# Kernel optimization log

Hardware: AMD Instinct MI355X
Metric: run time of the kernel (lower is better)

## Reference

```python
import jax, jax.numpy as jnp
import numpy as np

LS = 16000      # FFT length = ceil(L/stride)*stride with L=16000, stride=128
STRIDE = 128    # decimation hop
B, C, L, K = 32, 40, 16000, 128


def setup_inputs() -> dict:
    key = jax.random.key(0)
    k1, k2, k3 = jax.random.split(key, 3)
    x = jax.random.normal(k1, (B, 1, L), dtype=jnp.float32)
    kernels_real = jax.random.normal(k2, (C, K), dtype=jnp.float32)
    kernels_imag = jax.random.normal(k3, (C, K), dtype=jnp.float32)
    return {"x": x, "kernels_real": kernels_real, "kernels_imag": kernels_imag}


def reference(x, kernels_real, kernels_imag):
    # Complex analysis filters (C, K); zero-padded to LS inside fft via n=LS
    kernels = kernels_real + 1j * kernels_imag
    Xf = jnp.fft.fft(x, n=LS, axis=-1)                     # (B, 1, LS) complex
    Kf = jnp.fft.fft(kernels, n=LS, axis=-1)[None, :, :]   # (1, C, LS) complex
    y = jnp.fft.ifft(Xf * Kf, n=LS, axis=-1)               # (B, C, LS) circular conv
    return y[:, :, ::STRIDE]                               # (B, C, LS//STRIDE) complex
```

## Files before the change

kernel.cpp:

```cpp
#include <hip/hip_runtime.h>

#define BB     32
#define CC     40
#define LL     16000
#define KK     128
#define MM     125
#define KPAD   129
#define NOUT   (BB * CC * MM)

__global__ __launch_bounds__(256) void ISAC_conv_kernel(
    const float* __restrict__ x,
    const float* __restrict__ kr,
    const float* __restrict__ ki,
    float*       __restrict__ out,
    int mode)
{
    __shared__ unsigned int skc[CC * KPAD];

    for (int i = threadIdx.x; i < CC * KK; i += 256) {
        int c = i >> 7;
        int k = i & 127;
        unsigned int br = __float_as_uint(kr[i]);
        unsigned int bi = __float_as_uint(ki[i]);
        unsigned int hr = (br + 0x7FFFu + ((br >> 16) & 1u)) & 0xFFFF0000u;
        unsigned int hi = (bi + 0x7FFFu + ((bi >> 16) & 1u)) >> 16;
        skc[c * KPAD + k] = hr | hi;
    }
    __syncthreads();

    int id = blockIdx.x * 256 + threadIdx.x;
    int c  = id % CC;
    int t  = id / CC;
    int m  = t % MM;
    int b  = t / MM;

    const unsigned int* kc = skc + c * KPAD;
    const float*        xb = x + b * LL;
    const int base = m * KK;

    const float* p = xb + (m == 0 ? LL : base);

    unsigned int u0 = kc[0];
    float xv0  = xb[base];
    float accr = xv0 * __uint_as_float(u0 & 0xFFFF0000u);
    float acci = xv0 * __uint_as_float(u0 << 16);

#pragma unroll
    for (int j = 1; j < KK; ++j) {
        float        xv = p[-j];
        unsigned int u  = kc[j];
        accr = fmaf(xv, __uint_as_float(u & 0xFFFF0000u), accr);
        acci = fmaf(xv, __uint_as_float(u << 16),         acci);
    }

    int oidx = (b * CC + c) * MM + m;
    if (mode == 0) {
        out[oidx]        = accr;
        out[NOUT + oidx] = acci;
    } else if (mode == 1) {
        out[oidx] = accr;
    } else {
        reinterpret_cast<float2*>(out)[oidx] = make_float2(accr, acci);
    }
}

extern "C" void kernel_launch(void* const* d_in, const int* in_sizes, int n_in,
                              void* d_out, int out_size, void* d_ws, size_t ws_size,
                              hipStream_t stream) {
    const float* x  = (const float*)d_in[0];
    const float* kr = (const float*)d_in[1];
    const float* ki = (const float*)d_in[2];
    float* out = (float*)d_out;

    int mode;
    if (out_size == 2 * NOUT)      mode = 0;
    else if (out_size == NOUT)     mode = 1;
    else                           mode = 2;

    const int total = NOUT;
    const int block = 256;
    const int grid  = (total + block - 1) / block;

    ISAC_conv_kernel<<<grid, block, 0, stream>>>(x, kr, ki, out, mode);
}
```

Before: 62.72 us.

## Recast strided convolution as bf16 MFMA GEMM with hi/lo split of input

Adds a prep kernel that gathers each output's 128-sample window of x into a row matrix, splitting it into bf16 high and low parts, and packs both filter banks into a bf16 column matrix. A second kernel runs 16x16x32 bf16 MFMA tiles over these matrices and scatters results to the real and imaginary output planes. This replaces the per-thread scalar FMA loop with matrix-core work, at the cost of an extra kernel launch and workspace traffic. The path is taken only when the output is in split layout and enough workspace is provided.

```diff
diff --git a/kernel.cpp b/kernel.cpp
--- a/kernel.cpp
+++ b/kernel.cpp
@@ -7,6 +7,94 @@
 #define MM     125
 #define KPAD   129
 #define NOUT   (BB * CC * MM)
+#define RTOT   (BB * MM)
+#define NCOL   (2 * CC)
+#define NTILE  ((RTOT / 16) * (NCOL / 16))
+
+using short8 = __attribute__((ext_vector_type(8))) short;
+using f32x4  = __attribute__((ext_vector_type(4))) float;
+
+__device__ __forceinline__ unsigned int bf16_rne(float v) {
+    unsigned int u = __float_as_uint(v);
+    return (u + 0x7FFFu + ((u >> 16) & 1u)) >> 16;
+}
+
+__global__ __launch_bounds__(256) void ISAC_prep(
+    const float* __restrict__ x,
+    const float* __restrict__ kr,
+    const float* __restrict__ ki,
+    unsigned int* __restrict__ whi,
+    unsigned int* __restrict__ wlo,
+    unsigned int* __restrict__ wkb)
+{
+    int bid = blockIdx.x;
+    if (bid < 1000) {
+        int pid = bid * 256 + threadIdx.x;
+        int r  = pid >> 6;
+        int kp = pid & 63;
+        int b  = r / MM;
+        int m  = r - b * MM;
+        int i0 = m * KK - 2 * kp;  if (i0 < 0) i0 += LL;
+        int i1 = i0 - 1;           if (i1 < 0) i1 += LL;
+        float xa = x[b * LL + i0];
+        float xb = x[b * LL + i1];
+        unsigned int ha = bf16_rne(xa), hb = bf16_rne(xb);
+        float la = xa - __uint_as_float(ha << 16);
+        float lb = xb - __uint_as_float(hb << 16);
+        whi[pid] = ha | (hb << 16);
+        wlo[pid] = bf16_rne(la) | (bf16_rne(lb) << 16);
+    } else {
+        int pid = (bid - 1000) * 256 + threadIdx.x;
+        if (pid < NCOL * 64) {
+            int col = pid >> 6;
+            int kp  = pid & 63;
+            const float* src = (col < CC) ? (kr + col * KK) : (ki + (col - CC) * KK);
+            wkb[pid] = bf16_rne(src[2 * kp]) | (bf16_rne(src[2 * kp + 1]) << 16);
+        }
+    }
+}
+
+__global__ __launch_bounds__(256) void ISAC_gemm(
+    const unsigned short* __restrict__ whi,
+    const unsigned short* __restrict__ wlo,
+    const unsigned short* __restrict__ wkb,
+    float* __restrict__ out)
+{
+    int tile = blockIdx.x * 4 + (threadIdx.x >> 6);
+    if (tile >= NTILE) return;
+    int lane = threadIdx.x & 63;
+    int rt = tile / 5;
+    int ct = tile - rt * 5;
+    int row = lane & 15;
+    int g   = lane >> 4;
+
+    const short8* pa = (const short8*)(whi + ((rt * 16 + row) * KK + g * 8));
+    const short8* pl = (const short8*)(wlo + ((rt * 16 + row) * KK + g * 8));
+    const short8* pb = (const short8*)(wkb + ((ct * 16 + row) * KK + g * 8));
+
+    f32x4 acc = {0.f, 0.f, 0.f, 0.f};
+#pragma unroll
+    for (int ks = 0; ks < 4; ++ks) {
+        short8 ah = pa[ks * 4];
+        short8 al = pl[ks * 4];
+        short8 bv = pb[ks * 4];
+        acc = __builtin_amdgcn_mfma_f32_16x16x32_bf16(ah, bv, acc, 0, 0, 0);
+        acc = __builtin_amdgcn_mfma_f32_16x16x32_bf16(al, bv, acc, 0, 0, 0);
+    }
+
+    int colIdx = ct * 16 + row;
+    int rbase  = rt * 16 + g * 4;
+#pragma unroll
+    for (int e = 0; e < 4; ++e) {
+        int rr = rbase + e;
+        int b  = rr / MM;
+        int m  = rr - b * MM;
+        int oidx = (colIdx < CC)
+                 ? ((b * CC + colIdx) * MM + m)
+                 : (NOUT + (b * CC + (colIdx - CC)) * MM + m);
+        out[oidx] = acc[e];
+    }
+}
 
 __global__ __launch_bounds__(256) void ISAC_conv_kernel(
     const float* __restrict__ x,
@@ -37,7 +125,6 @@
     const unsigned int* kc = skc + c * KPAD;
     const float*        xb = x + b * LL;
     const int base = m * KK;
-
     const float* p = xb + (m == 0 ? LL : base);
 
     unsigned int u0 = kc[0];
@@ -77,9 +164,17 @@
     else if (out_size == NOUT)     mode = 1;
     else                           mode = 2;
 
-    const int total = NOUT;
-    const int block = 256;
-    const int grid  = (total + block - 1) / block;
-
-    ISAC_conv_kernel<<<grid, block, 0, stream>>>(x, kr, ki, out, mode);
+    const size_t ws_need = (size_t)(256000 + 256000 + 5120) * 4;
+    if (mode == 0 && d_ws != nullptr && ws_size >= ws_need) {
+        unsigned int* whi = (unsigned int*)d_ws;
+        unsigned int* wlo = whi + 256000;
+        unsigned int* wkb = wlo + 256000;
+        ISAC_prep<<<1020, 256, 0, stream>>>(x, kr, ki, whi, wlo, wkb);
+        ISAC_gemm<<<(NTILE + 3) / 4, 256, 0, stream>>>(
+            (const unsigned short*)whi, (const unsigned short*)wlo,
+            (const unsigned short*)wkb, out);
+    } else {
+        const int grid = (NOUT + 255) / 256;
+        ISAC_conv_kernel<<<grid, 256, 0, stream>>>(x, kr, ki, out, mode);
+    }
 }
```

Result: no change. 63.17 us (+0.7%).

## Compute strided convolution as bf16 MFMA GEMM with split-precision input

Applied to the files above, without the earlier changes.

Replaces the per-output scalar FMA loop with a matrix formulation: rows are (batch, output position) pairs and columns are the real and imaginary filter taps. Each wavefront computes a 16x16 tile with 16x16x32 bf16 MFMA instructions. The input signal is split into high and low bf16 parts to keep its precision, while the kernels are rounded to bf16 as before. This moves the work from vector ALUs to matrix cores and drops the shared-memory staging, at the cost of strided uncoalesced global loads and scattered output stores.

```diff
diff --git a/kernel.cpp b/kernel.cpp
--- a/kernel.cpp
+++ b/kernel.cpp
@@ -5,62 +5,103 @@
 #define LL     16000
 #define KK     128
 #define MM     125
-#define KPAD   129
 #define NOUT   (BB * CC * MM)
+#define RTOT   (BB * MM)
+#define NCOL   (2 * CC)
+#define NTILE  ((RTOT / 16) * (NCOL / 16))
 
-__global__ __launch_bounds__(256) void ISAC_conv_kernel(
+typedef short  short8  __attribute__((ext_vector_type(8)));
+typedef float  f32x4   __attribute__((ext_vector_type(4)));
+typedef unsigned int uint4v __attribute__((ext_vector_type(4)));
+
+__device__ __forceinline__ unsigned int bf16h(float f) {
+    unsigned int u = __float_as_uint(f);
+    return (u + 0x7FFFu + ((u >> 16) & 1u)) >> 16;
+}
+
+__global__ __launch_bounds__(256) void ISAC_fused(
     const float* __restrict__ x,
     const float* __restrict__ kr,
     const float* __restrict__ ki,
     float*       __restrict__ out,
     int mode)
 {
-    __shared__ unsigned int skc[CC * KPAD];
+    int tile = blockIdx.x * 4 + (threadIdx.x >> 6);
+    if (tile >= NTILE) return;
+    int lane = threadIdx.x & 63;
+    int rt   = tile / 5;
+    int ct   = tile - rt * 5;
+    int fr   = lane & 15;
+    int g    = lane >> 4;
 
-    for (int i = threadIdx.x; i < CC * KK; i += 256) {
-        int c = i >> 7;
-        int k = i & 127;
-        unsigned int br = __float_as_uint(kr[i]);
-        unsigned int bi = __float_as_uint(ki[i]);
-        unsigned int hr = (br + 0x7FFFu + ((br >> 16) & 1u)) & 0xFFFF0000u;
-        unsigned int hi = (bi + 0x7FFFu + ((bi >> 16) & 1u)) >> 16;
-        skc[c * KPAD + k] = hr | hi;
-    }
-    __syncthreads();
+    int r = rt * 16 + fr;
+    int b = r / MM;
+    int m = r - b * MM;
+    const float* xb = x + b * LL;
 
-    int id = blockIdx.x * 256 + threadIdx.x;
-    int c  = id % CC;
-    int t  = id / CC;
-    int m  = t % MM;
-    int b  = t / MM;
+    int col = ct * 16 + fr;
+    const float* kcol = (col < CC) ? (kr + col * KK) : (ki + (col - CC) * KK);
 
-    const unsigned int* kc = skc + c * KPAD;
-    const float*        xb = x + b * LL;
-    const int base = m * KK;
-
-    const float* p = xb + (m == 0 ? LL : base);
-
-    unsigned int u0 = kc[0];
-    float xv0  = xb[base];
-    float accr = xv0 * __uint_as_float(u0 & 0xFFFF0000u);
-    float acci = xv0 * __uint_as_float(u0 << 16);
+    f32x4 acc = {0.f, 0.f, 0.f, 0.f};
 
 #pragma unroll
-    for (int j = 1; j < KK; ++j) {
-        float        xv = p[-j];
-        unsigned int u  = kc[j];
-        accr = fmaf(xv, __uint_as_float(u & 0xFFFF0000u), accr);
-        acci = fmaf(xv, __uint_as_float(u << 16),         acci);
+    for (int ks = 0; ks < 4; ++ks) {
+        int kb = ks * 32 + g * 8;
+
+        float v[8];
+        if (m != 0) {
+            const float* p = xb + (m * KK - kb - 7);
+#pragma unroll
+            for (int i = 0; i < 8; ++i) v[i] = p[i];
+        } else {
+#pragma unroll
+            for (int i = 0; i < 8; ++i) {
+                int k = kb + 7 - i;
+                v[i] = xb[k == 0 ? 0 : (LL - k)];
+            }
+        }
+
+        unsigned int h[8], q[8];
+#pragma unroll
+        for (int e = 0; e < 8; ++e) {
+            float xe = v[7 - e];
+            h[e] = bf16h(xe);
+            float le = xe - __uint_as_float(h[e] << 16);
+            q[e] = bf16h(le);
+        }
+        uint4v ahu = { h[0] | (h[1] << 16), h[2] | (h[3] << 16),
+                       h[4] | (h[5] << 16), h[6] | (h[7] << 16) };
+        uint4v alu = { q[0] | (q[1] << 16), q[2] | (q[3] << 16),
+                       q[4] | (q[5] << 16), q[6] | (q[7] << 16) };
+
+        const float* pB = kcol + kb;
+        uint4v bvu = { bf16h(pB[0]) | (bf16h(pB[1]) << 16),
+                       bf16h(pB[2]) | (bf16h(pB[3]) << 16),
+                       bf16h(pB[4]) | (bf16h(pB[5]) << 16),
+                       bf16h(pB[6]) | (bf16h(pB[7]) << 16) };
+
+        short8 ah = __builtin_bit_cast(short8, ahu);
+        short8 al = __builtin_bit_cast(short8, alu);
+        short8 bv = __builtin_bit_cast(short8, bvu);
+        acc = __builtin_amdgcn_mfma_f32_16x16x32_bf16(ah, bv, acc, 0, 0, 0);
+        acc = __builtin_amdgcn_mfma_f32_16x16x32_bf16(al, bv, acc, 0, 0, 0);
     }
 
-    int oidx = (b * CC + c) * MM + m;
-    if (mode == 0) {
-        out[oidx]        = accr;
-        out[NOUT + oidx] = acci;
-    } else if (mode == 1) {
-        out[oidx] = accr;
-    } else {
-        reinterpret_cast<float2*>(out)[oidx] = make_float2(accr, acci);
+    int c  = (col < CC) ? col : (col - CC);
+#pragma unroll
+    for (int e = 0; e < 4; ++e) {
+        int rr = rt * 16 + g * 4 + e;
+        int ob = rr / MM;
+        int om = rr - ob * MM;
+        int oidx = (ob * CC + c) * MM + om;
+        float val = acc[e];
+        if (mode == 0) {
+            out[(col < CC ? 0 : NOUT) + oidx] = val;
+        } else if (mode == 2) {
+            out[2 * oidx + (col < CC ? 0 : 1)] = val;
+        } else if (col < CC) {
+            out[oidx] = val;
+        }
     }
 }
 
@@ -77,9 +118,6 @@
     else if (out_size == NOUT)     mode = 1;
     else                           mode = 2;
 
-    const int total = NOUT;
-    const int block = 256;
-    const int grid  = (total + block - 1) / block;
-
-    ISAC_conv_kernel<<<grid, block, 0, stream>>>(x, kr, ki, out, mode);
+    const int grid = (NTILE + 3) / 4;
+    ISAC_fused<<<grid, 256, 0, stream>>>(x, kr, ki, out, mode);
 }
```

Result: faster. 61.35 us (-2.2%).
